# Optimization experiments

Hardware: AMD Instinct MI355X
Metric: run time of the kernel (lower is better)

## Reference

```python
import jax, jax.numpy as jnp
import numpy as np

N_NODES = 100000   # number of graph nodes
N_EDGES = 1000000  # number of edges
D_IN = 64          # input feature dim
D_OUT = 64         # output feature dim
N_RELS = 16        # number of relation types


def setup_inputs() -> dict:
    key = jax.random.key(0)
    k1, k2, k3, k4, k5 = jax.random.split(key, 5)
    feat = jax.random.normal(k1, (N_NODES, D_IN), dtype=jnp.float32)
    weight = jax.random.normal(k2, (N_RELS, D_IN, D_OUT), dtype=jnp.float32) * 0.05
    src = jax.random.randint(k3, (N_EDGES,), 0, N_NODES)
    dst = jax.random.randint(k4, (N_EDGES,), 0, N_NODES)
    etypes = jax.random.randint(k5, (N_EDGES,), 0, N_RELS)
    return {"feat": feat, "weight": weight, "src": src, "dst": dst, "etypes": etypes}


def reference(feat, weight, src, dst, etypes):
    # gather source-node features per edge: h = edges.src['h']
    h = feat[src]                                # [E, d_in]
    n_rels = weight.shape[0]
    e, d_out = h.shape[0], weight.shape[2]

    # gather_mm(h, weight, idx_b=etypes): m_e = h_e @ weight[etypes_e]
    # grouped-GEMM realized as R masked dense GEMMs (R is small, fixed);
    # avoids materializing the [E, d_in, d_out] gathered weight tensor.
    def step(m, rw):
        r, w_r = rw
        mask = jnp.where(etypes == r, 1.0, 0.0).astype(h.dtype)  # [E]
        m = m + mask[:, None] * (h @ w_r)                        # [E, d_out]
        return m, None

    m0 = jnp.zeros((e, d_out), dtype=h.dtype)
    m, _ = jax.lax.scan(step, m0, (jnp.arange(n_rels), weight))

    # update_all(..., fn.sum('m', 'h')): scatter-sum messages to dst nodes
    out = jax.ops.segment_sum(m, dst, num_segments=feat.shape[0])  # [N, d_out]
    return out
```

## Files before the change

kernel.cpp:

```cpp
#include <hip/hip_runtime.h>
#include <hip/hip_bf16.h>
#include <stdint.h>

#define NNODES 100000
#define NEDGES 1000000
#define DIM 64
#define NRELS 16
#define EPB 2048
#define NB ((NEDGES + EPB - 1) / EPB)
#define PADCAP (NEDGES + NRELS * 64)
#define MAXTILES (PADCAP / 64)
#define NDN NNODES
#define BKT 256
#define NBKT ((NDN + BKT - 1) / BKT)

#define FEAT_BLKS 6250
#define W_BLKS 256
#define SETUP_BLKS (FEAT_BLKS + W_BLKS + NB)

#define WS_NEED 156943424ull

using short8  = __attribute__((ext_vector_type(8))) short;
using floatx4 = __attribute__((ext_vector_type(4))) float;
using uintx4  = __attribute__((ext_vector_type(4))) unsigned int;

__device__ __forceinline__ unsigned short f2bf(float f) {
    union { float f; uint32_t u; } v; v.f = f;
    uint32_t u = v.u;
    return (unsigned short)((u + 0x7FFFu + ((u >> 16) & 1u)) >> 16);
}
__device__ __forceinline__ float bf2f(uint32_t u16) {
    union { uint32_t u; float f; } v; v.u = u16 << 16;
    return v.f;
}
__device__ __forceinline__ uint32_t pk2(float a, float b) {
    __hip_bfloat162 h = __float22bfloat162_rn(make_float2(a, b));
    union { __hip_bfloat162 h; uint32_t u; } v; v.h = h;
    return v.u;
}

__global__ void k_setup(const float* __restrict__ feat, const float* __restrict__ W,
                        const int* __restrict__ et, const int* __restrict__ dst,
                        unsigned short* __restrict__ featB, unsigned short* __restrict__ Wt,
                        int* __restrict__ hist16, int* __restrict__ hist391) {
    __shared__ int cnt16[16];
    __shared__ int cnt391[NBKT];
    const int b = blockIdx.x;
    if (b < FEAT_BLKS) {
        int i = (b * 256 + threadIdx.x) * 4;
        const float4 f = *(const float4*)(feat + i);
        ushort4 o;
        o.x = f2bf(f.x); o.y = f2bf(f.y); o.z = f2bf(f.z); o.w = f2bf(f.w);
        *(ushort4*)(featB + i) = o;
    } else if (b < FEAT_BLKS + W_BLKS) {
        int t = (b - FEAT_BLKS) * 256 + threadIdx.x;
        int r = t >> 12, n = (t >> 6) & 63, k = t & 63;
        Wt[t] = f2bf(W[(r << 12) + (k << 6) + n]);
    } else {
        const int bb = b - (FEAT_BLKS + W_BLKS);
        if (threadIdx.x < 16) cnt16[threadIdx.x] = 0;
        for (int t = threadIdx.x; t < NBKT; t += 256) cnt391[t] = 0;
        __syncthreads();
        int start = bb * EPB;
        int end = min(NEDGES, start + EPB);
        for (int i = start + threadIdx.x; i < end; i += 256) {
            atomicAdd(&cnt16[et[i]], 1);
            atomicAdd(&cnt391[dst[i] >> 8], 1);
        }
        __syncthreads();
        if (threadIdx.x < 16) hist16[bb * 16 + threadIdx.x] = cnt16[threadIdx.x];
        for (int t = threadIdx.x; t < NBKT; t += 256)
            hist391[bb * NBKT + t] = cnt391[t];
    }
}

__global__ void k_scan(const int* __restrict__ hist, int* __restrict__ bbase,
                       int* __restrict__ Pve) {
    __shared__ int s_cnt[16];
    __shared__ int s_P[17];
    int w = threadIdx.x >> 6;
    int lane = threadIdx.x & 63;
    int carry = 0;
    for (int c = 0; c < NB; c += 64) {
        int idx = c + lane;
        int v = (idx < NB) ? hist[idx * 16 + w] : 0;
        int x = v;
        #pragma unroll
        for (int off = 1; off < 64; off <<= 1) {
            int y = __shfl_up(x, off);
            if (lane >= off) x += y;
        }
        if (idx < NB) bbase[idx * 16 + w] = carry + x - v;
        carry += __shfl(x, 63);
    }
    if (lane == 0) s_cnt[w] = carry;
    __syncthreads();
    if (threadIdx.x == 0) {
        int p = 0;
        for (int r = 0; r < 16; ++r) {
            s_P[r] = p;
            Pve[r] = p;
            Pve[17 + r] = p + s_cnt[r];
            p += (s_cnt[r] + 63) & ~63;
        }
        s_P[16] = p;
        Pve[16] = p;
    }
    __syncthreads();
    int pw = s_P[w];
    for (int idx = lane; idx < NB; idx += 64)
        bbase[idx * 16 + w] += pw;
}

__global__ void k_bscanA(const int* __restrict__ hist391, int* __restrict__ bbase391,
                         int* __restrict__ bstart) {
    int b = blockIdx.x * 4 + (threadIdx.x >> 6);
    int lane = threadIdx.x & 63;
    if (b >= NBKT) return;
    int carry = 0;
    for (int c = 0; c < NB; c += 64) {
        int idx = c + lane;
        int v = (idx < NB) ? hist391[idx * NBKT + b] : 0;
        int x = v;
        #pragma unroll
        for (int off = 1; off < 64; off <<= 1) {
            int y = __shfl_up(x, off);
            if (lane >= off) x += y;
        }
        if (idx < NB) bbase391[idx * NBKT + b] = carry + x - v;
        carry += __shfl(x, 63);
    }
    if (lane == 0) bstart[b] = carry;
}

__global__ void k_bscanB(int* __restrict__ bstart) {
    __shared__ int wtot[8];
    int t = threadIdx.x;
    int v = (t < NBKT) ? bstart[t] : 0;
    int lane = t & 63, w = t >> 6;
    int x = v;
    #pragma unroll
    for (int off = 1; off < 64; off <<= 1) {
        int y = __shfl_up(x, off);
        if (lane >= off) x += y;
    }
    if (lane == 63) wtot[w] = x;
    __syncthreads();
    int woff = 0;
    for (int i = 0; i < w; ++i) woff += wtot[i];
    if (t <= NBKT) {
        if (t < NBKT) bstart[t] = woff + x - v;
    }
    if (t == 511) {
        int total = 0;
        for (int i = 0; i < 8; ++i) total += wtot[i];
        bstart[NBKT] = total;
    }
}

__global__ void k_scatter(const int* __restrict__ et, const int* __restrict__ src,
                          const int* __restrict__ dst, const int* __restrict__ bbase16,
                          const int* __restrict__ bbase391, const int* __restrict__ bstart,
                          int2* __restrict__ pairE, unsigned short* __restrict__ dnode,
                          int buildPos) {
    __shared__ int base16[16];
    __shared__ int base391[NBKT];
    if (threadIdx.x < 16) base16[threadIdx.x] = bbase16[blockIdx.x * 16 + threadIdx.x];
    if (buildPos)
        for (int t = threadIdx.x; t < NBKT; t += 256)
            base391[t] = bbase391[blockIdx.x * NBKT + t] + bstart[t];
    __syncthreads();
    int start = blockIdx.x * EPB;
    int end = min(NEDGES, start + EPB);
    for (int i = start + threadIdx.x; i < end; i += 256) {
        int r = et[i];
        int pos = atomicAdd(&base16[r], 1);
        int d = dst[i];
        if (buildPos) {
            int bp = atomicAdd(&base391[d >> 8], 1);
            pairE[pos] = make_int2(src[i], bp);
            dnode[bp] = (unsigned short)(d & 255);
        } else {
            pairE[pos] = make_int2(src[i], d);
        }
    }
}

__global__ void __launch_bounds__(256)
k_bsort(const unsigned short* __restrict__ dnode, const int* __restrict__ bstart,
        int* __restrict__ remap, int* __restrict__ dnstart) {
    __shared__ int cnt[256];
    __shared__ int nodebase[256];
    __shared__ int wtot[4];
    const int b = blockIdx.x;
    const int start = bstart[b], end = bstart[b + 1];
    const int t = threadIdx.x;
    cnt[t] = 0;
    __syncthreads();
    for (int e = start + t; e < end; e += 256)
        atomicAdd(&cnt[dnode[e]], 1);
    __syncthreads();
    int v = cnt[t];
    int lane = t & 63, w = t >> 6;
    int x = v;
    #pragma unroll
    for (int off = 1; off < 64; off <<= 1) {
        int y = __shfl_up(x, off);
        if (lane >= off) x += y;
    }
    if (lane == 63) wtot[w] = x;
    __syncthreads();
    int woff = 0;
    for (int i = 0; i < w; ++i) woff += wtot[i];
    nodebase[t] = woff + x - v;
    cnt[t] = 0;
    __syncthreads();
    dnstart[b * 256 + t] = start + nodebase[t];
    for (int e = start + t; e < end; e += 256) {
        int node = dnode[e];
        int rk = atomicAdd(&cnt[node], 1);
        remap[e] = start + nodebase[node] + rk;
    }
}

__global__ void __launch_bounds__(256)
k_computeA(const unsigned short* __restrict__ featB,
           const unsigned short* __restrict__ Wt,
           const int2* __restrict__ pairE, const int* __restrict__ Pve,
           const int* __restrict__ remap,
           unsigned short* __restrict__ msgE) {
    __shared__ float lds[4][16 * 68];
    const int w = threadIdx.x >> 6;
    const int t = blockIdx.x * 4 + w;
    const int base = t * 64;
    const int total = Pve[16];
    if (base >= total) return;
    int r = 0;
    while (base >= Pve[r + 1]) ++r;
    const int validEnd = Pve[17 + r];
    const int lane = threadIdx.x & 63;
    const int quad = lane >> 4;
    const int l16 = lane & 15;

    const unsigned short* wr = Wt + (r << 12);
    short8 bfr[4][2];
    #pragma unroll
    for (int tn = 0; tn < 4; ++tn)
        #pragma unroll
        for (int ks = 0; ks < 2; ++ks)
            bfr[tn][ks] = *(const short8*)(wr + ((tn * 16 + l16) << 6) + ks * 32 + quad * 8);

    const int rr = lane >> 2, seg = lane & 3;
    #pragma unroll
    for (int tm = 0; tm < 4; ++tm) {
        int row = base + tm * 16 + l16;
        int s = (row < validEnd) ? pairE[row].x : 0;
        const unsigned short* fp = featB + (s << 6) + quad * 8;
        short8 a0 = *(const short8*)(fp);
        short8 a1 = *(const short8*)(fp + 32);
        #pragma unroll
        for (int tn = 0; tn < 4; ++tn) {
            floatx4 c = {0.f, 0.f, 0.f, 0.f};
            c = __builtin_amdgcn_mfma_f32_16x16x32_bf16(a0, bfr[tn][0], c, 0, 0, 0);
            c = __builtin_amdgcn_mfma_f32_16x16x32_bf16(a1, bfr[tn][1], c, 0, 0, 0);
            #pragma unroll
            for (int j = 0; j < 4; ++j)
                lds[w][(quad * 4 + j) * 68 + tn * 16 + l16] = c[j];
        }
        int rowi = base + tm * 16 + rr;
        int p = (rowi < validEnd) ? remap[pairE[rowi].y] : -1;
        if (p >= 0) {
            const float* lp = &lds[w][rr * 68 + seg * 16];
            uintx4 o0, o1;
            o0.x = pk2(lp[0],  lp[1]);  o0.y = pk2(lp[2],  lp[3]);
            o0.z = pk2(lp[4],  lp[5]);  o0.w = pk2(lp[6],  lp[7]);
            o1.x = pk2(lp[8],  lp[9]);  o1.y = pk2(lp[10], lp[11]);
            o1.z = pk2(lp[12], lp[13]); o1.w = pk2(lp[14], lp[15]);
            uintx4* op = (uintx4*)(msgE + (size_t)p * 64 + seg * 16);
            __builtin_nontemporal_store(o0, op);
            __builtin_nontemporal_store(o1, op + 1);
        }
    }
}

__global__ void __launch_bounds__(256)
k_reduce(const unsigned short* __restrict__ msgE,
         const int* __restrict__ dnstart, float* __restrict__ out) {
    int n = blockIdx.x * 4 + (threadIdx.x >> 6);
    if (n >= NDN) return;
    int lane = threadIdx.x & 63;
    int start = dnstart[n];
    int end = dnstart[n + 1];
    int c8 = (lane & 7) * 8;
    float a0 = 0.f, a1 = 0.f, a2 = 0.f, a3 = 0.f;
    float a4 = 0.f, a5 = 0.f, a6 = 0.f, a7 = 0.f;
    for (int row = start + (lane >> 3); row < end; row += 8) {
        uintx4 v = *(const uintx4*)(msgE + (size_t)row * 64 + c8);
        a0 += bf2f(v.x & 0xffffu); a1 += bf2f(v.x >> 16);
        a2 += bf2f(v.y & 0xffffu); a3 += bf2f(v.y >> 16);
        a4 += bf2f(v.z & 0xffffu); a5 += bf2f(v.z >> 16);
        a6 += bf2f(v.w & 0xffffu); a7 += bf2f(v.w >> 16);
    }
    #pragma unroll
    for (int m = 8; m <= 32; m <<= 1) {
        a0 += __shfl_xor(a0, m); a1 += __shfl_xor(a1, m);
        a2 += __shfl_xor(a2, m); a3 += __shfl_xor(a3, m);
        a4 += __shfl_xor(a4, m); a5 += __shfl_xor(a5, m);
        a6 += __shfl_xor(a6, m); a7 += __shfl_xor(a7, m);
    }
    if (lane < 8) {
        float* op = out + (size_t)n * 64 + lane * 8;
        *(float4*)(op)     = make_float4(a0, a1, a2, a3);
        *(float4*)(op + 4) = make_float4(a4, a5, a6, a7);
    }
}

__global__ void __launch_bounds__(256)
k_compute(const unsigned short* __restrict__ featB,
          const unsigned short* __restrict__ Wt,
          const int2* __restrict__ pairE, const int* __restrict__ Pve,
          float* __restrict__ out) {
    const int t = blockIdx.x * 4 + (threadIdx.x >> 6);
    const int base = t * 64;
    const int total = Pve[16];
    if (base >= total) return;
    int r = 0;
    while (base >= Pve[r + 1]) ++r;
    const int validEnd = Pve[17 + r];
    const int lane = threadIdx.x & 63;
    const int quad = lane >> 4;
    const int l16 = lane & 15;

    const unsigned short* wr = Wt + (r << 12);
    short8 bfr[4][2];
    #pragma unroll
    for (int tn = 0; tn < 4; ++tn)
        #pragma unroll
        for (int ks = 0; ks < 2; ++ks)
            bfr[tn][ks] = *(const short8*)(wr + ((tn * 16 + l16) << 6) + ks * 32 + quad * 8);

    #pragma unroll
    for (int tm = 0; tm < 4; ++tm) {
        int row = base + tm * 16 + l16;
        int s = (row < validEnd) ? pairE[row].x : 0;
        const unsigned short* fp = featB + (s << 6) + quad * 8;
        short8 a0 = *(const short8*)(fp);
        short8 a1 = *(const short8*)(fp + 32);
        floatx4 cc[4];
        #pragma unroll
        for (int tn = 0; tn < 4; ++tn) {
            floatx4 c = {0.f, 0.f, 0.f, 0.f};
            c = __builtin_amdgcn_mfma_f32_16x16x32_bf16(a0, bfr[tn][0], c, 0, 0, 0);
            c = __builtin_amdgcn_mfma_f32_16x16x32_bf16(a1, bfr[tn][1], c, 0, 0, 0);
            cc[tn] = c;
        }
        int pos0 = base + tm * 16 + quad * 4;
        #pragma unroll
        for (int j = 0; j < 4; ++j) {
            if (pos0 + j < validEnd) {
                int dn = pairE[pos0 + j].y;
                float* op = out + (dn << 6) + l16;
                #pragma unroll
                for (int tn = 0; tn < 4; ++tn)
                    atomicAdd(op + tn * 16, cc[tn][j]);
            }
        }
    }
}

extern "C" void kernel_launch(void* const* d_in, const int* in_sizes, int n_in,
                              void* d_out, int out_size, void* d_ws, size_t ws_size,
                              hipStream_t stream) {
    const float* feat = (const float*)d_in[0];
    const float* W    = (const float*)d_in[1];
    const int* src    = (const int*)d_in[2];
    const int* dst    = (const int*)d_in[3];
    const int* et     = (const int*)d_in[4];
    float* out = (float*)d_out;
    char* ws = (char*)d_ws;

    unsigned short* featB = (unsigned short*)(ws);
    unsigned short* Wt    = (unsigned short*)(ws + 12800000);
    int* hist16   = (int*)(ws + 12931072);
    int* bbase16  = (int*)(ws + 12963840);
    int* Pve      = (int*)(ws + 12996608);
    int* hist391  = (int*)(ws + 12996864);
    int* bbase391 = (int*)(ws + 13764864);
    int* bstart   = (int*)(ws + 14532864);
    unsigned short* dnode = (unsigned short*)(ws + 14534464);
    int* dnstart  = (int*)(ws + 16534464);
    int* remap    = (int*)(ws + 16935232);
    int2* pairE   = (int2*)(ws + 20935232);
    unsigned short* msgE = (unsigned short*)(ws + 28943424);

    const int usePhases = (ws_size >= WS_NEED) ? 1 : 0;

    k_setup<<<SETUP_BLKS, 256, 0, stream>>>(feat, W, et, dst, featB, Wt, hist16, hist391);
    k_scan<<<1, 1024, 0, stream>>>(hist16, bbase16, Pve);

    if (usePhases) {
        k_bscanA<<<(NBKT + 3) / 4, 256, 0, stream>>>(hist391, bbase391, bstart);
        k_bscanB<<<1, 512, 0, stream>>>(bstart);
        k_scatter<<<NB, 256, 0, stream>>>(et, src, dst, bbase16, bbase391, bstart,
                                          pairE, dnode, 1);
        k_bsort<<<NBKT, 256, 0, stream>>>(dnode, bstart, remap, dnstart);
        k_computeA<<<(MAXTILES + 3) / 4, 256, 0, stream>>>(featB, Wt, pairE, Pve,
                                                           remap, msgE);
        k_reduce<<<(NDN + 3) / 4, 256, 0, stream>>>(msgE, dnstart, out);
    } else {
        hipMemsetAsync(d_out, 0, (size_t)out_size * sizeof(float), stream);
        k_scatter<<<NB, 256, 0, stream>>>(et, src, dst, bbase16, bbase391, bstart,
                                          pairE, dnode, 0);
        k_compute<<<(MAXTILES + 3) / 4, 256, 0, stream>>>(featB, Wt, pairE, Pve, out);
    }
}
```

Before: 241.9 us.

## Precompute per-relation node transforms and gather by destination instead of per-edge GEMM

Replaces the relation-sorted per-edge GEMM with a dense transform of every node by all 16 relation weights into a bf16 table, then each destination node gathers rows keyed by (src, relation). This removes the relation histogram/scan/sort and the per-edge message buffer. In exchange it multiplies GEMM work by the edge/node ratio mismatch and writes a ~200MB table read randomly, and raises workspace needs, with a new scalar fp32 fallback path.

New measurement: 312.8 us. 29.3% more time.

```diff
diff --git a/kernel.cpp b/kernel.cpp
--- a/kernel.cpp
+++ b/kernel.cpp
@@ -4,21 +4,18 @@
 
 #define NNODES 100000
 #define NEDGES 1000000
-#define DIM 64
 #define NRELS 16
 #define EPB 2048
 #define NB ((NEDGES + EPB - 1) / EPB)
-#define PADCAP (NEDGES + NRELS * 64)
-#define MAXTILES (PADCAP / 64)
-#define NDN NNODES
 #define BKT 256
-#define NBKT ((NDN + BKT - 1) / BKT)
+#define NBKT ((NNODES + BKT - 1) / BKT)
+#define NTILES (NNODES / 16)
 
 #define FEAT_BLKS 6250
 #define W_BLKS 256
 #define SETUP_BLKS (FEAT_BLKS + W_BLKS + NB)
 
-#define WS_NEED 156943424ull
+#define WS_NEED 229670016ull
 
 using short8  = __attribute__((ext_vector_type(8))) short;
 using floatx4 = __attribute__((ext_vector_type(4))) float;
@@ -40,10 +37,9 @@
 }
 
 __global__ void k_setup(const float* __restrict__ feat, const float* __restrict__ W,
-                        const int* __restrict__ et, const int* __restrict__ dst,
+                        const int* __restrict__ dst,
                         unsigned short* __restrict__ featB, unsigned short* __restrict__ Wt,
-                        int* __restrict__ hist16, int* __restrict__ hist391) {
-    __shared__ int cnt16[16];
+                        int* __restrict__ hist391) {
     __shared__ int cnt391[NBKT];
     const int b = blockIdx.x;
     if (b < FEAT_BLKS) {
@@ -58,64 +54,23 @@
         Wt[t] = f2bf(W[(r << 12) + (k << 6) + n]);
     } else {
         const int bb = b - (FEAT_BLKS + W_BLKS);
-        if (threadIdx.x < 16) cnt16[threadIdx.x] = 0;
         for (int t = threadIdx.x; t < NBKT; t += 256) cnt391[t] = 0;
         __syncthreads();
         int start = bb * EPB;
         int end = min(NEDGES, start + EPB);
-        for (int i = start + threadIdx.x; i < end; i += 256) {
-            atomicAdd(&cnt16[et[i]], 1);
+        for (int i = start + threadIdx.x; i < end; i += 256)
             atomicAdd(&cnt391[dst[i] >> 8], 1);
-        }
         __syncthreads();
-        if (threadIdx.x < 16) hist16[bb * 16 + threadIdx.x] = cnt16[threadIdx.x];
         for (int t = threadIdx.x; t < NBKT; t += 256)
             hist391[bb * NBKT + t] = cnt391[t];
     }
 }
 
-__global__ void k_scan(const int* __restrict__ hist, int* __restrict__ bbase,
-                       int* __restrict__ Pve) {
-    __shared__ int s_cnt[16];
-    __shared__ int s_P[17];
-    int w = threadIdx.x >> 6;
-    int lane = threadIdx.x & 63;
-    int carry = 0;
-    for (int c = 0; c < NB; c += 64) {
-        int idx = c + lane;
-        int v = (idx < NB) ? hist[idx * 16 + w] : 0;
-        int x = v;
-        #pragma unroll
-        for (int off = 1; off < 64; off <<= 1) {
-            int y = __shfl_up(x, off);
-            if (lane >= off) x += y;
-        }
-        if (idx < NB) bbase[idx * 16 + w] = carry + x - v;
-        carry += __shfl(x, 63);
-    }
-    if (lane == 0) s_cnt[w] = carry;
-    __syncthreads();
-    if (threadIdx.x == 0) {
-        int p = 0;
-        for (int r = 0; r < 16; ++r) {
-            s_P[r] = p;
-            Pve[r] = p;
-            Pve[17 + r] = p + s_cnt[r];
-            p += (s_cnt[r] + 63) & ~63;
-        }
-        s_P[16] = p;
-        Pve[16] = p;
-    }
-    __syncthreads();
-    int pw = s_P[w];
-    for (int idx = lane; idx < NB; idx += 64)
-        bbase[idx * 16 + w] += pw;
-}
-
-__global__ void k_bscanA(const int* __restrict__ hist391, int* __restrict__ bbase391,
-                         int* __restrict__ bstart) {
-    int b = blockIdx.x * 4 + (threadIdx.x >> 6);
-    int lane = threadIdx.x & 63;
+__global__ void __launch_bounds__(1024)
+k_bscanA(const int* __restrict__ hist391, int* __restrict__ bbase391,
+         int* __restrict__ bstart) {
+    int w = threadIdx.x >> 6, lane = threadIdx.x & 63;
+    int b = blockIdx.x * 16 + w;
     if (b >= NBKT) return;
     int carry = 0;
     for (int c = 0; c < NB; c += 64) {
@@ -148,9 +103,7 @@
     __syncthreads();
     int woff = 0;
     for (int i = 0; i < w; ++i) woff += wtot[i];
-    if (t <= NBKT) {
-        if (t < NBKT) bstart[t] = woff + x - v;
-    }
+    if (t < NBKT) bstart[t] = woff + x - v;
     if (t == 511) {
         int total = 0;
         for (int i = 0; i < 8; ++i) total += wtot[i];
@@ -159,36 +112,27 @@
 }
 
 __global__ void k_scatter(const int* __restrict__ et, const int* __restrict__ src,
-                          const int* __restrict__ dst, const int* __restrict__ bbase16,
+                          const int* __restrict__ dst,
                           const int* __restrict__ bbase391, const int* __restrict__ bstart,
-                          int2* __restrict__ pairE, unsigned short* __restrict__ dnode,
-                          int buildPos) {
-    __shared__ int base16[16];
+                          int* __restrict__ keyE, unsigned short* __restrict__ dnode) {
     __shared__ int base391[NBKT];
-    if (threadIdx.x < 16) base16[threadIdx.x] = bbase16[blockIdx.x * 16 + threadIdx.x];
-    if (buildPos)
-        for (int t = threadIdx.x; t < NBKT; t += 256)
-            base391[t] = bbase391[blockIdx.x * NBKT + t] + bstart[t];
+    for (int t = threadIdx.x; t < NBKT; t += 256)
+        base391[t] = bbase391[blockIdx.x * NBKT + t] + bstart[t];
     __syncthreads();
     int start = blockIdx.x * EPB;
     int end = min(NEDGES, start + EPB);
     for (int i = start + threadIdx.x; i < end; i += 256) {
-        int r = et[i];
-        int pos = atomicAdd(&base16[r], 1);
         int d = dst[i];
-        if (buildPos) {
-            int bp = atomicAdd(&base391[d >> 8], 1);
-            pairE[pos] = make_int2(src[i], bp);
-            dnode[bp] = (unsigned short)(d & 255);
-        } else {
-            pairE[pos] = make_int2(src[i], d);
-        }
-    }
-}
-
-__global__ void __launch_bounds__(256)
-k_bsort(const unsigned short* __restrict__ dnode, const int* __restrict__ bstart,
-        int* __restrict__ remap, int* __restrict__ dnstart) {
+        int bp = atomicAdd(&base391[d >> 8], 1);
+        keyE[bp] = src[i] | (et[i] << 17);
+        dnode[bp] = (unsigned short)(d & 255);
+    }
+}
+
+__global__ void __launch_bounds__(256)
+k_bsort(const unsigned short* __restrict__ dnode, const int* __restrict__ keyE,
+        const int* __restrict__ bstart,
+        int* __restrict__ keyS, int* __restrict__ dnstart) {
     __shared__ int cnt[256];
     __shared__ int nodebase[256];
     __shared__ int wtot[4];
@@ -216,78 +160,59 @@
     cnt[t] = 0;
     __syncthreads();
     dnstart[b * 256 + t] = start + nodebase[t];
+    if (b == NBKT - 1 && t == 255) dnstart[NBKT * 256] = end;
     for (int e = start + t; e < end; e += 256) {
         int node = dnode[e];
         int rk = atomicAdd(&cnt[node], 1);
-        remap[e] = start + nodebase[node] + rk;
-    }
-}
-
-__global__ void __launch_bounds__(256)
-k_computeA(const unsigned short* __restrict__ featB,
-           const unsigned short* __restrict__ Wt,
-           const int2* __restrict__ pairE, const int* __restrict__ Pve,
-           const int* __restrict__ remap,
-           unsigned short* __restrict__ msgE) {
+        keyS[start + nodebase[node] + rk] = keyE[e];
+    }
+}
+
+__global__ void __launch_bounds__(256)
+k_tf(const unsigned short* __restrict__ featB, const unsigned short* __restrict__ Wt,
+     unsigned short* __restrict__ tfeat) {
     __shared__ float lds[4][16 * 68];
     const int w = threadIdx.x >> 6;
-    const int t = blockIdx.x * 4 + w;
-    const int base = t * 64;
-    const int total = Pve[16];
-    if (base >= total) return;
-    int r = 0;
-    while (base >= Pve[r + 1]) ++r;
-    const int validEnd = Pve[17 + r];
+    const int tile = blockIdx.x * 4 + w;
+    if (tile >= NTILES) return;
+    const int base = tile * 16;
     const int lane = threadIdx.x & 63;
-    const int quad = lane >> 4;
-    const int l16 = lane & 15;
-
-    const unsigned short* wr = Wt + (r << 12);
-    short8 bfr[4][2];
-    #pragma unroll
-    for (int tn = 0; tn < 4; ++tn)
-        #pragma unroll
-        for (int ks = 0; ks < 2; ++ks)
-            bfr[tn][ks] = *(const short8*)(wr + ((tn * 16 + l16) << 6) + ks * 32 + quad * 8);
-
+    const int quad = lane >> 4, l16 = lane & 15;
+    const unsigned short* fp = featB + (size_t)(base + l16) * 64 + quad * 8;
+    short8 a0 = *(const short8*)(fp);
+    short8 a1 = *(const short8*)(fp + 32);
     const int rr = lane >> 2, seg = lane & 3;
-    #pragma unroll
-    for (int tm = 0; tm < 4; ++tm) {
-        int row = base + tm * 16 + l16;
-        int s = (row < validEnd) ? pairE[row].x : 0;
-        const unsigned short* fp = featB + (s << 6) + quad * 8;
-        short8 a0 = *(const short8*)(fp);
-        short8 a1 = *(const short8*)(fp + 32);
+    for (int rel = 0; rel < NRELS; ++rel) {
+        const unsigned short* wr = Wt + (rel << 12);
         #pragma unroll
         for (int tn = 0; tn < 4; ++tn) {
+            const unsigned short* bp = wr + ((tn * 16 + l16) << 6) + quad * 8;
+            short8 b0 = *(const short8*)(bp);
+            short8 b1 = *(const short8*)(bp + 32);
             floatx4 c = {0.f, 0.f, 0.f, 0.f};
-            c = __builtin_amdgcn_mfma_f32_16x16x32_bf16(a0, bfr[tn][0], c, 0, 0, 0);
-            c = __builtin_amdgcn_mfma_f32_16x16x32_bf16(a1, bfr[tn][1], c, 0, 0, 0);
+            c = __builtin_amdgcn_mfma_f32_16x16x32_bf16(a0, b0, c, 0, 0, 0);
+            c = __builtin_amdgcn_mfma_f32_16x16x32_bf16(a1, b1, c, 0, 0, 0);
             #pragma unroll
             for (int j = 0; j < 4; ++j)
                 lds[w][(quad * 4 + j) * 68 + tn * 16 + l16] = c[j];
         }
-        int rowi = base + tm * 16 + rr;
-        int p = (rowi < validEnd) ? remap[pairE[rowi].y] : -1;
-        if (p >= 0) {
-            const float* lp = &lds[w][rr * 68 + seg * 16];
-            uintx4 o0, o1;
-            o0.x = pk2(lp[0],  lp[1]);  o0.y = pk2(lp[2],  lp[3]);
-            o0.z = pk2(lp[4],  lp[5]);  o0.w = pk2(lp[6],  lp[7]);
-            o1.x = pk2(lp[8],  lp[9]);  o1.y = pk2(lp[10], lp[11]);
-            o1.z = pk2(lp[12], lp[13]); o1.w = pk2(lp[14], lp[15]);
-            uintx4* op = (uintx4*)(msgE + (size_t)p * 64 + seg * 16);
-            __builtin_nontemporal_store(o0, op);
-            __builtin_nontemporal_store(o1, op + 1);
-        }
-    }
-}
-
-__global__ void __launch_bounds__(256)
-k_reduce(const unsigned short* __restrict__ msgE,
+        const float* lp = &lds[w][rr * 68 + seg * 16];
+        uintx4 o0, o1;
+        o0.x = pk2(lp[0],  lp[1]);  o0.y = pk2(lp[2],  lp[3]);
+        o0.z = pk2(lp[4],  lp[5]);  o0.w = pk2(lp[6],  lp[7]);
+        o1.x = pk2(lp[8],  lp[9]);  o1.y = pk2(lp[10], lp[11]);
+        o1.z = pk2(lp[12], lp[13]); o1.w = pk2(lp[14], lp[15]);
+        unsigned short* op = tfeat + ((size_t)rel * NNODES + base + rr) * 64 + seg * 16;
+        __builtin_nontemporal_store(o0, (uintx4*)op);
+        __builtin_nontemporal_store(o1, (uintx4*)op + 1);
+    }
+}
+
+__global__ void __launch_bounds__(256)
+k_gather(const unsigned short* __restrict__ tfeat, const int* __restrict__ keyS,
          const int* __restrict__ dnstart, float* __restrict__ out) {
     int n = blockIdx.x * 4 + (threadIdx.x >> 6);
-    if (n >= NDN) return;
+    if (n >= NNODES) return;
     int lane = threadIdx.x & 63;
     int start = dnstart[n];
     int end = dnstart[n + 1];
@@ -295,7 +220,10 @@
     float a0 = 0.f, a1 = 0.f, a2 = 0.f, a3 = 0.f;
     float a4 = 0.f, a5 = 0.f, a6 = 0.f, a7 = 0.f;
     for (int row = start + (lane >> 3); row < end; row += 8) {
-        uintx4 v = *(const uintx4*)(msgE + (size_t)row * 64 + c8);
+        int key = keyS[row];
+        int s = key & 0x1FFFF, rel = key >> 17;
+        const uintx4* p = (const uintx4*)(tfeat + ((size_t)rel * NNODES + s) * 64 + c8);
+        uintx4 v = *p;
         a0 += bf2f(v.x & 0xffffu); a1 += bf2f(v.x >> 16);
         a2 += bf2f(v.y & 0xffffu); a3 += bf2f(v.y >> 16);
         a4 += bf2f(v.z & 0xffffu); a5 += bf2f(v.z >> 16);
@@ -316,56 +244,18 @@
 }
 
 __global__ void __launch_bounds__(256)
-k_compute(const unsigned short* __restrict__ featB,
-          const unsigned short* __restrict__ Wt,
-          const int2* __restrict__ pairE, const int* __restrict__ Pve,
-          float* __restrict__ out) {
-    const int t = blockIdx.x * 4 + (threadIdx.x >> 6);
-    const int base = t * 64;
-    const int total = Pve[16];
-    if (base >= total) return;
-    int r = 0;
-    while (base >= Pve[r + 1]) ++r;
-    const int validEnd = Pve[17 + r];
-    const int lane = threadIdx.x & 63;
-    const int quad = lane >> 4;
-    const int l16 = lane & 15;
-
-    const unsigned short* wr = Wt + (r << 12);
-    short8 bfr[4][2];
-    #pragma unroll
-    for (int tn = 0; tn < 4; ++tn)
-        #pragma unroll
-        for (int ks = 0; ks < 2; ++ks)
-            bfr[tn][ks] = *(const short8*)(wr + ((tn * 16 + l16) << 6) + ks * 32 + quad * 8);
-
-    #pragma unroll
-    for (int tm = 0; tm < 4; ++tm) {
-        int row = base + tm * 16 + l16;
-        int s = (row < validEnd) ? pairE[row].x : 0;
-        const unsigned short* fp = featB + (s << 6) + quad * 8;
-        short8 a0 = *(const short8*)(fp);
-        short8 a1 = *(const short8*)(fp + 32);
-        floatx4 cc[4];
-        #pragma unroll
-        for (int tn = 0; tn < 4; ++tn) {
-            floatx4 c = {0.f, 0.f, 0.f, 0.f};
-            c = __builtin_amdgcn_mfma_f32_16x16x32_bf16(a0, bfr[tn][0], c, 0, 0, 0);
-            c = __builtin_amdgcn_mfma_f32_16x16x32_bf16(a1, bfr[tn][1], c, 0, 0, 0);
-            cc[tn] = c;
-        }
-        int pos0 = base + tm * 16 + quad * 4;
-        #pragma unroll
-        for (int j = 0; j < 4; ++j) {
-            if (pos0 + j < validEnd) {
-                int dn = pairE[pos0 + j].y;
-                float* op = out + (dn << 6) + l16;
-                #pragma unroll
-                for (int tn = 0; tn < 4; ++tn)
-                    atomicAdd(op + tn * 16, cc[tn][j]);
-            }
-        }
-    }
+k_fb(const float* __restrict__ feat, const float* __restrict__ W,
+     const int* __restrict__ src, const int* __restrict__ dst,
+     const int* __restrict__ et, float* __restrict__ out) {
+    int e = blockIdx.x * 4 + (threadIdx.x >> 6);
+    if (e >= NEDGES) return;
+    int c = threadIdx.x & 63;
+    int s = src[e], d = dst[e], r = et[e];
+    const float* fr = feat + (size_t)s * 64;
+    const float* wr = W + ((size_t)r << 12);
+    float acc = 0.f;
+    for (int k = 0; k < 64; ++k) acc += fr[k] * wr[k * 64 + c];
+    atomicAdd(out + (size_t)d * 64 + c, acc);
 }
 
 extern "C" void kernel_launch(void* const* d_in, const int* in_sizes, int n_in,
@@ -381,36 +271,25 @@
 
     unsigned short* featB = (unsigned short*)(ws);
     unsigned short* Wt    = (unsigned short*)(ws + 12800000);
-    int* hist16   = (int*)(ws + 12931072);
-    int* bbase16  = (int*)(ws + 12963840);
-    int* Pve      = (int*)(ws + 12996608);
-    int* hist391  = (int*)(ws + 12996864);
-    int* bbase391 = (int*)(ws + 13764864);
-    int* bstart   = (int*)(ws + 14532864);
-    unsigned short* dnode = (unsigned short*)(ws + 14534464);
-    int* dnstart  = (int*)(ws + 16534464);
-    int* remap    = (int*)(ws + 16935232);
-    int2* pairE   = (int2*)(ws + 20935232);
-    unsigned short* msgE = (unsigned short*)(ws + 28943424);
-
-    const int usePhases = (ws_size >= WS_NEED) ? 1 : 0;
-
-    k_setup<<<SETUP_BLKS, 256, 0, stream>>>(feat, W, et, dst, featB, Wt, hist16, hist391);
-    k_scan<<<1, 1024, 0, stream>>>(hist16, bbase16, Pve);
-
-    if (usePhases) {
-        k_bscanA<<<(NBKT + 3) / 4, 256, 0, stream>>>(hist391, bbase391, bstart);
+    int* hist391  = (int*)(ws + 12931072);
+    int* bbase391 = (int*)(ws + 13699072);
+    int* bstart   = (int*)(ws + 14467072);
+    unsigned short* dnode = (unsigned short*)(ws + 14469120);
+    int* dnstart  = (int*)(ws + 16469120);
+    int* keyE     = (int*)(ws + 16870016);
+    int* keyS     = (int*)(ws + 20870016);
+    unsigned short* tfeat = (unsigned short*)(ws + 24870016);
+
+    if (ws_size >= WS_NEED) {
+        k_setup<<<SETUP_BLKS, 256, 0, stream>>>(feat, W, dst, featB, Wt, hist391);
+        k_bscanA<<<(NBKT + 15) / 16, 1024, 0, stream>>>(hist391, bbase391, bstart);
         k_bscanB<<<1, 512, 0, stream>>>(bstart);
-        k_scatter<<<NB, 256, 0, stream>>>(et, src, dst, bbase16, bbase391, bstart,
-                                          pairE, dnode, 1);
-        k_bsort<<<NBKT, 256, 0, stream>>>(dnode, bstart, remap, dnstart);
-        k_computeA<<<(MAXTILES + 3) / 4, 256, 0, stream>>>(featB, Wt, pairE, Pve,
-                                                           remap, msgE);
-        k_reduce<<<(NDN + 3) / 4, 256, 0, stream>>>(msgE, dnstart, out);
+        k_scatter<<<NB, 256, 0, stream>>>(et, src, dst, bbase391, bstart, keyE, dnode);
+        k_bsort<<<NBKT, 256, 0, stream>>>(dnode, keyE, bstart, keyS, dnstart);
+        k_tf<<<(NTILES + 3) / 4, 256, 0, stream>>>(featB, Wt, tfeat);
+        k_gather<<<(NNODES + 3) / 4, 256, 0, stream>>>(tfeat, keyS, dnstart, out);
     } else {
         hipMemsetAsync(d_out, 0, (size_t)out_size * sizeof(float), stream);
-        k_scatter<<<NB, 256, 0, stream>>>(et, src, dst, bbase16, bbase391, bstart,
-                                          pairE, dnode, 0);
-        k_compute<<<(MAXTILES + 3) / 4, 256, 0, stream>>>(featB, Wt, pairE, Pve, out);
-    }
-}
+        k_fb<<<(NEDGES + 3) / 4, 256, 0, stream>>>(feat, W, src, dst, et, out);
+    }
+}
```

## Write messages contiguously by relation order and gather them in reduce via sorted keys

Applied to the files above, without the earlier changes.

The compute kernel now writes bf16 messages sequentially in relation-sorted order instead of scattering them to destination-sorted positions. The reduce kernel gathers each message through a destination-sorted key array built in the bucket sort. The two histogram scans are merged into one launch, and the fallback path is replaced with a simple per-edge kernel. This trades scattered writes in compute for indexed reads in reduce, and removes the remap indirection.

Result: faster. 235.3 us (-2.7%).

```diff
diff --git a/kernel.cpp b/kernel.cpp
--- a/kernel.cpp
+++ b/kernel.cpp
@@ -4,7 +4,6 @@
 
 #define NNODES 100000
 #define NEDGES 1000000
-#define DIM 64
 #define NRELS 16
 #define EPB 2048
 #define NB ((NEDGES + EPB - 1) / EPB)
@@ -17,8 +16,9 @@
 #define FEAT_BLKS 6250
 #define W_BLKS 256
 #define SETUP_BLKS (FEAT_BLKS + W_BLKS + NB)
-
-#define WS_NEED 156943424ull
+#define SCANS_BLKS (1 + (NBKT + 15) / 16)
+
+#define WS_NEED 157070848ull
 
 using short8  = __attribute__((ext_vector_type(8))) short;
 using floatx4 = __attribute__((ext_vector_type(4))) float;
@@ -74,63 +74,64 @@
     }
 }
 
-__global__ void k_scan(const int* __restrict__ hist, int* __restrict__ bbase,
-                       int* __restrict__ Pve) {
-    __shared__ int s_cnt[16];
-    __shared__ int s_P[17];
+__global__ void __launch_bounds__(1024)
+k_scans(const int* __restrict__ hist16, int* __restrict__ bbase16,
+        int* __restrict__ Pve,
+        const int* __restrict__ hist391, int* __restrict__ bbase391,
+        int* __restrict__ bstart) {
     int w = threadIdx.x >> 6;
     int lane = threadIdx.x & 63;
-    int carry = 0;
-    for (int c = 0; c < NB; c += 64) {
-        int idx = c + lane;
-        int v = (idx < NB) ? hist[idx * 16 + w] : 0;
-        int x = v;
-        #pragma unroll
-        for (int off = 1; off < 64; off <<= 1) {
-            int y = __shfl_up(x, off);
-            if (lane >= off) x += y;
-        }
-        if (idx < NB) bbase[idx * 16 + w] = carry + x - v;
-        carry += __shfl(x, 63);
-    }
-    if (lane == 0) s_cnt[w] = carry;
-    __syncthreads();
-    if (threadIdx.x == 0) {
-        int p = 0;
-        for (int r = 0; r < 16; ++r) {
-            s_P[r] = p;
-            Pve[r] = p;
-            Pve[17 + r] = p + s_cnt[r];
-            p += (s_cnt[r] + 63) & ~63;
-        }
-        s_P[16] = p;
-        Pve[16] = p;
-    }
-    __syncthreads();
-    int pw = s_P[w];
-    for (int idx = lane; idx < NB; idx += 64)
-        bbase[idx * 16 + w] += pw;
-}
-
-__global__ void k_bscanA(const int* __restrict__ hist391, int* __restrict__ bbase391,
-                         int* __restrict__ bstart) {
-    int b = blockIdx.x * 4 + (threadIdx.x >> 6);
-    int lane = threadIdx.x & 63;
-    if (b >= NBKT) return;
-    int carry = 0;
-    for (int c = 0; c < NB; c += 64) {
-        int idx = c + lane;
-        int v = (idx < NB) ? hist391[idx * NBKT + b] : 0;
-        int x = v;
-        #pragma unroll
-        for (int off = 1; off < 64; off <<= 1) {
-            int y = __shfl_up(x, off);
-            if (lane >= off) x += y;
-        }
-        if (idx < NB) bbase391[idx * NBKT + b] = carry + x - v;
-        carry += __shfl(x, 63);
-    }
-    if (lane == 0) bstart[b] = carry;
+    if (blockIdx.x == 0) {
+        __shared__ int s_cnt[16];
+        __shared__ int s_P[17];
+        int carry = 0;
+        for (int c = 0; c < NB; c += 64) {
+            int idx = c + lane;
+            int v = (idx < NB) ? hist16[idx * 16 + w] : 0;
+            int x = v;
+            #pragma unroll
+            for (int off = 1; off < 64; off <<= 1) {
+                int y = __shfl_up(x, off);
+                if (lane >= off) x += y;
+            }
+            if (idx < NB) bbase16[idx * 16 + w] = carry + x - v;
+            carry += __shfl(x, 63);
+        }
+        if (lane == 0) s_cnt[w] = carry;
+        __syncthreads();
+        if (threadIdx.x == 0) {
+            int p = 0;
+            for (int r = 0; r < 16; ++r) {
+                s_P[r] = p;
+                Pve[r] = p;
+                Pve[17 + r] = p + s_cnt[r];
+                p += (s_cnt[r] + 63) & ~63;
+            }
+            s_P[16] = p;
+            Pve[16] = p;
+        }
+        __syncthreads();
+        int pw = s_P[w];
+        for (int idx = lane; idx < NB; idx += 64)
+            bbase16[idx * 16 + w] += pw;
+    } else {
+        int b = (blockIdx.x - 1) * 16 + w;
+        if (b >= NBKT) return;
+        int carry = 0;
+        for (int c = 0; c < NB; c += 64) {
+            int idx = c + lane;
+            int v = (idx < NB) ? hist391[idx * NBKT + b] : 0;
+            int x = v;
+            #pragma unroll
+            for (int off = 1; off < 64; off <<= 1) {
+                int y = __shfl_up(x, off);
+                if (lane >= off) x += y;
+            }
+            if (idx < NB) bbase391[idx * NBKT + b] = carry + x - v;
+            carry += __shfl(x, 63);
+        }
+        if (lane == 0) bstart[b] = carry;
+    }
 }
 
 __global__ void k_bscanB(int* __restrict__ bstart) {
@@ -148,9 +149,7 @@
     __syncthreads();
     int woff = 0;
     for (int i = 0; i < w; ++i) woff += wtot[i];
-    if (t <= NBKT) {
-        if (t < NBKT) bstart[t] = woff + x - v;
-    }
+    if (t < NBKT) bstart[t] = woff + x - v;
     if (t == 511) {
         int total = 0;
         for (int i = 0; i < 8; ++i) total += wtot[i];
@@ -161,34 +160,31 @@
 __global__ void k_scatter(const int* __restrict__ et, const int* __restrict__ src,
                           const int* __restrict__ dst, const int* __restrict__ bbase16,
                           const int* __restrict__ bbase391, const int* __restrict__ bstart,
-                          int2* __restrict__ pairE, unsigned short* __restrict__ dnode,
-                          int buildPos) {
+                          int* __restrict__ srcS, int* __restrict__ keyE,
+                          unsigned short* __restrict__ dnode) {
     __shared__ int base16[16];
     __shared__ int base391[NBKT];
     if (threadIdx.x < 16) base16[threadIdx.x] = bbase16[blockIdx.x * 16 + threadIdx.x];
-    if (buildPos)
-        for (int t = threadIdx.x; t < NBKT; t += 256)
-            base391[t] = bbase391[blockIdx.x * NBKT + t] + bstart[t];
+    for (int t = threadIdx.x; t < NBKT; t += 256)
+        base391[t] = bbase391[blockIdx.x * NBKT + t] + bstart[t];
     __syncthreads();
     int start = blockIdx.x * EPB;
     int end = min(NEDGES, start + EPB);
     for (int i = start + threadIdx.x; i < end; i += 256) {
         int r = et[i];
         int pos = atomicAdd(&base16[r], 1);
+        srcS[pos] = src[i];
         int d = dst[i];
-        if (buildPos) {
-            int bp = atomicAdd(&base391[d >> 8], 1);
-            pairE[pos] = make_int2(src[i], bp);
-            dnode[bp] = (unsigned short)(d & 255);
-        } else {
-            pairE[pos] = make_int2(src[i], d);
-        }
+        int bp = atomicAdd(&base391[d >> 8], 1);
+        keyE[bp] = pos;
+        dnode[bp] = (unsigned short)(d & 255);
     }
 }
 
 __global__ void __launch_bounds__(256)
-k_bsort(const unsigned short* __restrict__ dnode, const int* __restrict__ bstart,
-        int* __restrict__ remap, int* __restrict__ dnstart) {
+k_bsort(const unsigned short* __restrict__ dnode, const int* __restrict__ keyE,
+        const int* __restrict__ bstart,
+        int* __restrict__ keyS, int* __restrict__ dnstart) {
     __shared__ int cnt[256];
     __shared__ int nodebase[256];
     __shared__ int wtot[4];
@@ -216,18 +212,18 @@
     cnt[t] = 0;
     __syncthreads();
     dnstart[b * 256 + t] = start + nodebase[t];
+    if (b == NBKT - 1 && t == 255) dnstart[NBKT * 256] = end;
     for (int e = start + t; e < end; e += 256) {
         int node = dnode[e];
         int rk = atomicAdd(&cnt[node], 1);
-        remap[e] = start + nodebase[node] + rk;
+        keyS[start + nodebase[node] + rk] = keyE[e];
     }
 }
 
 __global__ void __launch_bounds__(256)
 k_computeA(const unsigned short* __restrict__ featB,
            const unsigned short* __restrict__ Wt,
-           const int2* __restrict__ pairE, const int* __restrict__ Pve,
-           const int* __restrict__ remap,
+           const int* __restrict__ srcS, const int* __restrict__ Pve,
            unsigned short* __restrict__ msgE) {
     __shared__ float lds[4][16 * 68];
     const int w = threadIdx.x >> 6;
@@ -254,7 +250,7 @@
     #pragma unroll
     for (int tm = 0; tm < 4; ++tm) {
         int row = base + tm * 16 + l16;
-        int s = (row < validEnd) ? pairE[row].x : 0;
+        int s = (row < validEnd) ? srcS[row] : 0;
         const unsigned short* fp = featB + (s << 6) + quad * 8;
         short8 a0 = *(const short8*)(fp);
         short8 a1 = *(const short8*)(fp + 32);
@@ -267,24 +263,21 @@
             for (int j = 0; j < 4; ++j)
                 lds[w][(quad * 4 + j) * 68 + tn * 16 + l16] = c[j];
         }
-        int rowi = base + tm * 16 + rr;
-        int p = (rowi < validEnd) ? remap[pairE[rowi].y] : -1;
-        if (p >= 0) {
-            const float* lp = &lds[w][rr * 68 + seg * 16];
-            uintx4 o0, o1;
-            o0.x = pk2(lp[0],  lp[1]);  o0.y = pk2(lp[2],  lp[3]);
-            o0.z = pk2(lp[4],  lp[5]);  o0.w = pk2(lp[6],  lp[7]);
-            o1.x = pk2(lp[8],  lp[9]);  o1.y = pk2(lp[10], lp[11]);
-            o1.z = pk2(lp[12], lp[13]); o1.w = pk2(lp[14], lp[15]);
-            uintx4* op = (uintx4*)(msgE + (size_t)p * 64 + seg * 16);
-            __builtin_nontemporal_store(o0, op);
-            __builtin_nontemporal_store(o1, op + 1);
-        }
+        int grow = base + tm * 16 + rr;
+        const float* lp = &lds[w][rr * 68 + seg * 16];
+        uintx4 o0, o1;
+        o0.x = pk2(lp[0],  lp[1]);  o0.y = pk2(lp[2],  lp[3]);
+        o0.z = pk2(lp[4],  lp[5]);  o0.w = pk2(lp[6],  lp[7]);
+        o1.x = pk2(lp[8],  lp[9]);  o1.y = pk2(lp[10], lp[11]);
+        o1.z = pk2(lp[12], lp[13]); o1.w = pk2(lp[14], lp[15]);
+        uintx4* op = (uintx4*)(msgE + (size_t)grow * 64 + seg * 16);
+        op[0] = o0;
+        op[1] = o1;
     }
 }
 
 __global__ void __launch_bounds__(256)
-k_reduce(const unsigned short* __restrict__ msgE,
+k_reduce(const unsigned short* __restrict__ msgE, const int* __restrict__ keyS,
          const int* __restrict__ dnstart, float* __restrict__ out) {
     int n = blockIdx.x * 4 + (threadIdx.x >> 6);
     if (n >= NDN) return;
@@ -295,7 +288,8 @@
     float a0 = 0.f, a1 = 0.f, a2 = 0.f, a3 = 0.f;
     float a4 = 0.f, a5 = 0.f, a6 = 0.f, a7 = 0.f;
     for (int row = start + (lane >> 3); row < end; row += 8) {
-        uintx4 v = *(const uintx4*)(msgE + (size_t)row * 64 + c8);
+        int rp = keyS[row];
+        uintx4 v = *(const uintx4*)(msgE + (size_t)rp * 64 + c8);
         a0 += bf2f(v.x & 0xffffu); a1 += bf2f(v.x >> 16);
         a2 += bf2f(v.y & 0xffffu); a3 += bf2f(v.y >> 16);
         a4 += bf2f(v.z & 0xffffu); a5 += bf2f(v.z >> 16);
@@ -316,56 +310,18 @@
 }
 
 __global__ void __launch_bounds__(256)
-k_compute(const unsigned short* __restrict__ featB,
-          const unsigned short* __restrict__ Wt,
-          const int2* __restrict__ pairE, const int* __restrict__ Pve,
-          float* __restrict__ out) {
-    const int t = blockIdx.x * 4 + (threadIdx.x >> 6);
-    const int base = t * 64;
-    const int total = Pve[16];
-    if (base >= total) return;
-    int r = 0;
-    while (base >= Pve[r + 1]) ++r;
-    const int validEnd = Pve[17 + r];
-    const int lane = threadIdx.x & 63;
-    const int quad = lane >> 4;
-    const int l16 = lane & 15;
-
-    const unsigned short* wr = Wt + (r << 12);
-    short8 bfr[4][2];
-    #pragma unroll
-    for (int tn = 0; tn < 4; ++tn)
-        #pragma unroll
-        for (int ks = 0; ks < 2; ++ks)
-            bfr[tn][ks] = *(const short8*)(wr + ((tn * 16 + l16) << 6) + ks * 32 + quad * 8);
-
-    #pragma unroll
-    for (int tm = 0; tm < 4; ++tm) {
-        int row = base + tm * 16 + l16;
-        int s = (row < validEnd) ? pairE[row].x : 0;
-        const unsigned short* fp = featB + (s << 6) + quad * 8;
-        short8 a0 = *(const short8*)(fp);
-        short8 a1 = *(const short8*)(fp + 32);
-        floatx4 cc[4];
-        #pragma unroll
-        for (int tn = 0; tn < 4; ++tn) {
-            floatx4 c = {0.f, 0.f, 0.f, 0.f};
-            c = __builtin_amdgcn_mfma_f32_16x16x32_bf16(a0, bfr[tn][0], c, 0, 0, 0);
-            c = __builtin_amdgcn_mfma_f32_16x16x32_bf16(a1, bfr[tn][1], c, 0, 0, 0);
-            cc[tn] = c;
-        }
-        int pos0 = base + tm * 16 + quad * 4;
-        #pragma unroll
-        for (int j = 0; j < 4; ++j) {
-            if (pos0 + j < validEnd) {
-                int dn = pairE[pos0 + j].y;
-                float* op = out + (dn << 6) + l16;
-                #pragma unroll
-                for (int tn = 0; tn < 4; ++tn)
-                    atomicAdd(op + tn * 16, cc[tn][j]);
-            }
-        }
-    }
+k_fb(const float* __restrict__ feat, const float* __restrict__ W,
+     const int* __restrict__ src, const int* __restrict__ dst,
+     const int* __restrict__ et, float* __restrict__ out) {
+    int e = blockIdx.x * 4 + (threadIdx.x >> 6);
+    if (e >= NEDGES) return;
+    int c = threadIdx.x & 63;
+    int s = src[e], d = dst[e], r = et[e];
+    const float* fr = feat + (size_t)s * 64;
+    const float* wr = W + ((size_t)r << 12);
+    float acc = 0.f;
+    for (int k = 0; k < 64; ++k) acc += fr[k] * wr[k * 64 + c];
+    atomicAdd(out + (size_t)d * 64 + c, acc);
 }
 
 extern "C" void kernel_launch(void* const* d_in, const int* in_sizes, int n_in,
@@ -387,30 +343,26 @@
     int* hist391  = (int*)(ws + 12996864);
     int* bbase391 = (int*)(ws + 13764864);
     int* bstart   = (int*)(ws + 14532864);
-    unsigned short* dnode = (unsigned short*)(ws + 14534464);
-    int* dnstart  = (int*)(ws + 16534464);
-    int* remap    = (int*)(ws + 16935232);
-    int2* pairE   = (int2*)(ws + 20935232);
-    unsigned short* msgE = (unsigned short*)(ws + 28943424);
-
-    const int usePhases = (ws_size >= WS_NEED) ? 1 : 0;
-
-    k_setup<<<SETUP_BLKS, 256, 0, stream>>>(feat, W, et, dst, featB, Wt, hist16, hist391);
-    k_scan<<<1, 1024, 0, stream>>>(hist16, bbase16, Pve);
-
-    if (usePhases) {
-        k_bscanA<<<(NBKT + 3) / 4, 256, 0, stream>>>(hist391, bbase391, bstart);
+    unsigned short* dnode = (unsigned short*)(ws + 14534912);
+    int* dnstart  = (int*)(ws + 16534912);
+    int* keyE     = (int*)(ws + 16935680);
+    int* keyS     = (int*)(ws + 20935680);
+    int* srcS     = (int*)(ws + 24935680);
+    unsigned short* msgE = (unsigned short*)(ws + 28939776);
+
+    if (ws_size >= WS_NEED) {
+        k_setup<<<SETUP_BLKS, 256, 0, stream>>>(feat, W, et, dst, featB, Wt,
+                                                hist16, hist391);
+        k_scans<<<SCANS_BLKS, 1024, 0, stream>>>(hist16, bbase16, Pve, hist391,
+                                                 bbase391, bstart);
         k_bscanB<<<1, 512, 0, stream>>>(bstart);
         k_scatter<<<NB, 256, 0, stream>>>(et, src, dst, bbase16, bbase391, bstart,
-                                          pairE, dnode, 1);
-        k_bsort<<<NBKT, 256, 0, stream>>>(dnode, bstart, remap, dnstart);
-        k_computeA<<<(MAXTILES + 3) / 4, 256, 0, stream>>>(featB, Wt, pairE, Pve,
-                                                           remap, msgE);
-        k_reduce<<<(NDN + 3) / 4, 256, 0, stream>>>(msgE, dnstart, out);
+                                          srcS, keyE, dnode);
+        k_bsort<<<NBKT, 256, 0, stream>>>(dnode, keyE, bstart, keyS, dnstart);
+        k_computeA<<<(MAXTILES + 3) / 4, 256, 0, stream>>>(featB, Wt, srcS, Pve, msgE);
+        k_reduce<<<(NDN + 3) / 4, 256, 0, stream>>>(msgE, keyS, dnstart, out);
     } else {
         hipMemsetAsync(d_out, 0, (size_t)out_size * sizeof(float), stream);
-        k_scatter<<<NB, 256, 0, stream>>>(et, src, dst, bbase16, bbase391, bstart,
-                                          pairE, dnode, 0);
-        k_compute<<<(MAXTILES + 3) / 4, 256, 0, stream>>>(featB, Wt, pairE, Pve, out);
-    }
-}
+        k_fb<<<(NEDGES + 3) / 4, 256, 0, stream>>>(feat, W, src, dst, et, out);
+    }
+}
```
